# Kernel tuning notes

Measured on AMD Instinct MI355X. Metric: run time of the kernel, lower is better.

Reference implementation:

```python
import jax, jax.numpy as jnp
import numpy as np

ALPHA = 0.2          # LeakyReLU negative slope
WIN = 100            # window_size
D_EMBED = 2 * WIN    # default d_embed doubled in __init__


def setup_inputs() -> dict:
    key = jax.random.key(0)
    k1, k2, k3, k4 = jax.random.split(key, 4)
    B, W, F = 16, WIN, 128
    inp = jax.random.normal(k1, (B, W, F), dtype=jnp.float32)
    # linear: in=2*window_size, out=d_embed (stored as [in, out] for x @ W)
    lim = np.sqrt(1.0 / (2 * WIN))
    lin_w = jax.random.uniform(k2, (2 * WIN, D_EMBED), jnp.float32, -lim, lim)
    lin_b = jax.random.uniform(k3, (D_EMBED,), jnp.float32, -lim, lim)
    # attention vector w: [d_embed] (xavier on [d_embed,1])
    glim = np.sqrt(6.0 / (D_EMBED + 1))
    attn_w = jax.random.uniform(k4, (D_EMBED,), jnp.float32, -glim, glim)
    return {"input": inp, "lin_w": lin_w, "lin_b": lin_b, "attn_w": attn_w}


def reference(input, lin_w, lin_b, attn_w):
    # input: [B, window, features] -> x: [B, K, window] (K = features = nodes)
    x = jnp.transpose(input, (0, 2, 1))
    # Split the linear over the concat: linear(cat(xi, xj)) = xi@W1 + xj@W2 + b
    W1, W2 = lin_w[:WIN], lin_w[WIN:]          # each [window, d_embed]
    left = jnp.einsum("bkw,wd->bkd", x, W1)    # [B, K, d]
    right = jnp.einsum("bkw,wd->bkd", x, W2)   # [B, K, d]
    pre = left[:, :, None, :] + right[:, None, :, :] + lin_b  # [B, K, K, d]
    act = jnp.where(pre >= 0, pre, ALPHA * pre)                # LeakyReLU
    e = jnp.einsum("bijd,d->bij", act, attn_w)                 # [B, K, K]
    attention = jax.nn.softmax(e, axis=2)
    # dropout p=0.0 (eval/identity)
    h = jax.nn.sigmoid(jnp.einsum("bij,bjw->biw", attention, x))  # [B, K, window]
    return jnp.transpose(h, (0, 2, 1))  # [B, window, K]
```

## Files before the change

### kernel.cpp

```cpp
#include <hip/hip_runtime.h>

#define ALPHA 0.2f
#define BATCH 16
#define WIN 100
#define KN 128
#define DE 200
#define IT 8

typedef float v2f __attribute__((ext_vector_type(2)));

__global__ __launch_bounds__(256) void k_lin(
    const float* __restrict__ in, const float* __restrict__ lw,
    const float* __restrict__ lb, float* __restrict__ Rt, float* __restrict__ Lt) {
  int blk = blockIdx.x;
  int b = blk / 25, dt = blk % 25;
  int t = threadIdx.x;
  int j = t & (KN - 1);
  int dbase = __builtin_amdgcn_readfirstlane(dt * 8 + (t >> 7) * 4);
  const float* inb = in + (size_t)b * WIN * KN + j;
  const float* lwl = lw + dbase;
  const float* lwr = lw + WIN * DE + dbase;
  float la0 = 0, la1 = 0, la2 = 0, la3 = 0;
  float ra0 = 0, ra1 = 0, ra2 = 0, ra3 = 0;
#pragma unroll 10
  for (int w = 0; w < WIN; ++w) {
    float x = inb[w * KN];
    float4 wl = *reinterpret_cast<const float4*>(lwl + w * DE);
    float4 wr = *reinterpret_cast<const float4*>(lwr + w * DE);
    la0 = fmaf(x, wl.x, la0); la1 = fmaf(x, wl.y, la1);
    la2 = fmaf(x, wl.z, la2); la3 = fmaf(x, wl.w, la3);
    ra0 = fmaf(x, wr.x, ra0); ra1 = fmaf(x, wr.y, ra1);
    ra2 = fmaf(x, wr.z, ra2); ra3 = fmaf(x, wr.w, ra3);
  }
  float4 bb = *reinterpret_cast<const float4*>(lb + dbase);
  float* rp = Rt + ((size_t)b * DE + dbase) * KN + j;
  float* lp = Lt + ((size_t)b * DE + dbase) * KN + j;
  rp[0 * KN] = ra0 + bb.x; rp[1 * KN] = ra1 + bb.y;
  rp[2 * KN] = ra2 + bb.z; rp[3 * KN] = ra3 + bb.w;
  lp[0 * KN] = la0; lp[1 * KN] = la1; lp[2 * KN] = la2; lp[3 * KN] = la3;
}

__global__ __launch_bounds__(1024) void k_attn_out(
    const float* __restrict__ in, const float* __restrict__ aw,
    const float* __restrict__ Rt, const float* __restrict__ Lt,
    float* __restrict__ out) {
  int blk = blockIdx.x;
  int b = blk >> 4, it = blk & 15;
  int i0 = it * IT;
  int t = threadIdx.x;
  __shared__ float part[8][IT][KN];
  __shared__ float part_r[8][KN];
  __shared__ float ats[IT][132];

  {
    int j = t & (KN - 1);
    int db = __builtin_amdgcn_readfirstlane((t >> 7) * 25);
    int dh = t >> 7;
    const float* rtb = Rt + (size_t)b * DE * KN + j;
    const float* ltb = Lt + (size_t)b * DE * KN + i0;
    v2f acc0 = 0.f, acc1 = 0.f, acc2 = 0.f, acc3 = 0.f;
    float racc = 0.f;
#pragma unroll 5
    for (int dd = 0; dd < 25; ++dd) {
      int d = db + dd;
      float r = rtb[(size_t)d * KN];
      float a = aw[d];
      float4 L0 = *reinterpret_cast<const float4*>(ltb + (size_t)d * KN);
      float4 L1 = *reinterpret_cast<const float4*>(ltb + (size_t)d * KN + 4);
      racc = fmaf(r, a, racc);
      v2f rv = {r, r}, av = {a, a}, z = 0.f;
      v2f p0 = (v2f){L0.x, L0.y} + rv;
      v2f p1 = (v2f){L0.z, L0.w} + rv;
      v2f p2 = (v2f){L1.x, L1.y} + rv;
      v2f p3 = (v2f){L1.z, L1.w} + rv;
      p0 = __builtin_elementwise_min(p0, z);
      p1 = __builtin_elementwise_min(p1, z);
      p2 = __builtin_elementwise_min(p2, z);
      p3 = __builtin_elementwise_min(p3, z);
      acc0 += p0 * av; acc1 += p1 * av; acc2 += p2 * av; acc3 += p3 * av;
    }
    part[dh][0][j] = acc0.x; part[dh][1][j] = acc0.y;
    part[dh][2][j] = acc1.x; part[dh][3][j] = acc1.y;
    part[dh][4][j] = acc2.x; part[dh][5][j] = acc2.y;
    part[dh][6][j] = acc3.x; part[dh][7][j] = acc3.y;
    part_r[dh][j] = racc;
  }
  __syncthreads();

  {
    int wid = t >> 6;
    if (wid < IT) {
      int r = wid, l = t & 63;
      float ra0 = 0.f, ra1 = 0.f, m0 = 0.f, m1 = 0.f;
#pragma unroll
      for (int dh = 0; dh < 8; ++dh) {
        ra0 += part_r[dh][l];     ra1 += part_r[dh][l + 64];
        m0  += part[dh][r][l];    m1  += part[dh][r][l + 64];
      }
      float e0 = fmaf(m0, -(1.f - ALPHA), ra0);
      float e1 = fmaf(m1, -(1.f - ALPHA), ra1);
      float m = fmaxf(e0, e1);
      for (int off = 32; off; off >>= 1) m = fmaxf(m, __shfl_xor(m, off));
      float p0 = __expf(e0 - m), p1 = __expf(e1 - m);
      float s = p0 + p1;
      for (int off = 32; off; off >>= 1) s += __shfl_xor(s, off);
      float inv = 1.f / s;
      ats[r][l] = p0 * inv;
      ats[r][l + 64] = p1 * inv;
    }
  }
  __syncthreads();

  if (t < 4 * WIN) {
    int w = t >> 2, q = t & 3;
    const float* xw = in + ((size_t)b * WIN + w) * KN;
    const float* a0p = &ats[q * 2][0];
    const float* a1p = &ats[q * 2 + 1][0];
    float s0 = 0.f, s1 = 0.f;
#pragma unroll 8
    for (int j = 0; j < KN; j += 4) {
      float4 x4 = *reinterpret_cast<const float4*>(xw + j);
      float4 aa = *reinterpret_cast<const float4*>(a0p + j);
      float4 ab = *reinterpret_cast<const float4*>(a1p + j);
      s0 = fmaf(aa.x, x4.x, s0); s0 = fmaf(aa.y, x4.y, s0);
      s0 = fmaf(aa.z, x4.z, s0); s0 = fmaf(aa.w, x4.w, s0);
      s1 = fmaf(ab.x, x4.x, s1); s1 = fmaf(ab.y, x4.y, s1);
      s1 = fmaf(ab.z, x4.z, s1); s1 = fmaf(ab.w, x4.w, s1);
    }
    float o0 = 1.f / (1.f + __expf(-s0));
    float o1 = 1.f / (1.f + __expf(-s1));
    *reinterpret_cast<float2*>(&out[((size_t)b * WIN + w) * KN + i0 + q * 2]) =
        make_float2(o0, o1);
  }
}

extern "C" void kernel_launch(void* const* d_in, const int* in_sizes, int n_in,
                              void* d_out, int out_size, void* d_ws, size_t ws_size,
                              hipStream_t stream) {
  const float* in = (const float*)d_in[0];
  const float* lw = (const float*)d_in[1];
  const float* lb = (const float*)d_in[2];
  const float* aw = (const float*)d_in[3];
  float* out = (float*)d_out;

  float* Rt = (float*)d_ws;
  float* Lt = Rt + (size_t)BATCH * DE * KN;

  k_lin     <<<BATCH * 25, 256, 0, stream>>>(in, lw, lb, Rt, Lt);
  k_attn_out<<<BATCH * 16, 1024, 0, stream>>>(in, aw, Rt, Lt, out);
}
```

Measured before the change: 22.90 us.

## Split linear reduction across more threads and widen output stage parallelism

The linear kernel now runs 1024 threads per block. Each thread computes 2 output dims over half of the window, and the two partial sums are combined through shared memory before the stores. The attention kernel's d-loop is fully unrolled, and the output stage uses 800 threads computing one output each instead of 400 threads computing two. The goal is more threads in flight and shorter serial dependency chains, paid for with an extra shared-memory reduction and barrier, plus scalar stores in place of float2 stores.

Result: slower. 47.50 us (+107.4%).

```diff
diff --git a/kernel.cpp b/kernel.cpp
--- a/kernel.cpp
+++ b/kernel.cpp
@@ -9,35 +9,41 @@
 
 typedef float v2f __attribute__((ext_vector_type(2)));
 
-__global__ __launch_bounds__(256) void k_lin(
+__global__ __launch_bounds__(1024) void k_lin(
     const float* __restrict__ in, const float* __restrict__ lw,
     const float* __restrict__ lb, float* __restrict__ Rt, float* __restrict__ Lt) {
   int blk = blockIdx.x;
   int b = blk / 25, dt = blk % 25;
   int t = threadIdx.x;
   int j = t & (KN - 1);
-  int dbase = __builtin_amdgcn_readfirstlane(dt * 8 + (t >> 7) * 4);
-  const float* inb = in + (size_t)b * WIN * KN + j;
-  const float* lwl = lw + dbase;
-  const float* lwr = lw + WIN * DE + dbase;
-  float la0 = 0, la1 = 0, la2 = 0, la3 = 0;
-  float ra0 = 0, ra1 = 0, ra2 = 0, ra3 = 0;
-#pragma unroll 10
-  for (int w = 0; w < WIN; ++w) {
-    float x = inb[w * KN];
-    float4 wl = *reinterpret_cast<const float4*>(lwl + w * DE);
-    float4 wr = *reinterpret_cast<const float4*>(lwr + w * DE);
+  int g = t >> 7;
+  int dh = g & 3, wh = g >> 2;
+  int dp = __builtin_amdgcn_readfirstlane(dt * 8 + dh * 2);
+  __shared__ float pl[2][8][KN];
+  __shared__ float pr[2][8][KN];
+
+  const float* xp = in + ((size_t)b * WIN + wh * 50) * KN + j;
+  const float* lwl = lw + (size_t)(wh * 50) * DE + dp;
+  const float* lwr = lw + (size_t)(WIN + wh * 50) * DE + dp;
+  float la0 = 0, la1 = 0, ra0 = 0, ra1 = 0;
+#pragma unroll 25
+  for (int k = 0; k < 50; ++k) {
+    float x = xp[(size_t)k * KN];
+    float2 wl = *reinterpret_cast<const float2*>(lwl + (size_t)k * DE);
+    float2 wr = *reinterpret_cast<const float2*>(lwr + (size_t)k * DE);
     la0 = fmaf(x, wl.x, la0); la1 = fmaf(x, wl.y, la1);
-    la2 = fmaf(x, wl.z, la2); la3 = fmaf(x, wl.w, la3);
     ra0 = fmaf(x, wr.x, ra0); ra1 = fmaf(x, wr.y, ra1);
-    ra2 = fmaf(x, wr.z, ra2); ra3 = fmaf(x, wr.w, ra3);
   }
-  float4 bb = *reinterpret_cast<const float4*>(lb + dbase);
-  float* rp = Rt + ((size_t)b * DE + dbase) * KN + j;
-  float* lp = Lt + ((size_t)b * DE + dbase) * KN + j;
-  rp[0 * KN] = ra0 + bb.x; rp[1 * KN] = ra1 + bb.y;
-  rp[2 * KN] = ra2 + bb.z; rp[3 * KN] = ra3 + bb.w;
-  lp[0 * KN] = la0; lp[1 * KN] = la1; lp[2 * KN] = la2; lp[3 * KN] = la3;
+  pl[wh][dh * 2][j] = la0; pl[wh][dh * 2 + 1][j] = la1;
+  pr[wh][dh * 2][j] = ra0; pr[wh][dh * 2 + 1][j] = ra1;
+  __syncthreads();
+
+  int d8 = t >> 7;
+  int d = dt * 8 + d8;
+  float lsum = pl[0][d8][j] + pl[1][d8][j];
+  float rsum = pr[0][d8][j] + pr[1][d8][j] + lb[d];
+  Lt[((size_t)b * DE + d) * KN + j] = lsum;
+  Rt[((size_t)b * DE + d) * KN + j] = rsum;
 }
 
 __global__ __launch_bounds__(1024) void k_attn_out(
@@ -54,13 +60,13 @@
 
   {
     int j = t & (KN - 1);
-    int db = __builtin_amdgcn_readfirstlane((t >> 7) * 25);
     int dh = t >> 7;
+    int db = __builtin_amdgcn_readfirstlane(dh * 25);
     const float* rtb = Rt + (size_t)b * DE * KN + j;
     const float* ltb = Lt + (size_t)b * DE * KN + i0;
     v2f acc0 = 0.f, acc1 = 0.f, acc2 = 0.f, acc3 = 0.f;
     float racc = 0.f;
-#pragma unroll 5
+#pragma unroll 25
     for (int dd = 0; dd < 25; ++dd) {
       int d = db + dd;
       float r = rtb[(size_t)d * KN];
@@ -111,26 +117,19 @@
   }
   __syncthreads();
 
-  if (t < 4 * WIN) {
-    int w = t >> 2, q = t & 3;
+  if (t < 8 * WIN) {
+    int w = t >> 3, q = t & 7;
     const float* xw = in + ((size_t)b * WIN + w) * KN;
-    const float* a0p = &ats[q * 2][0];
-    const float* a1p = &ats[q * 2 + 1][0];
-    float s0 = 0.f, s1 = 0.f;
+    const float* ap = &ats[q][0];
+    float s = 0.f;
 #pragma unroll 8
-    for (int j = 0; j < KN; j += 4) {
-      float4 x4 = *reinterpret_cast<const float4*>(xw + j);
-      float4 aa = *reinterpret_cast<const float4*>(a0p + j);
-      float4 ab = *reinterpret_cast<const float4*>(a1p + j);
-      s0 = fmaf(aa.x, x4.x, s0); s0 = fmaf(aa.y, x4.y, s0);
-      s0 = fmaf(aa.z, x4.z, s0); s0 = fmaf(aa.w, x4.w, s0);
-      s1 = fmaf(ab.x, x4.x, s1); s1 = fmaf(ab.y, x4.y, s1);
-      s1 = fmaf(ab.z, x4.z, s1); s1 = fmaf(ab.w, x4.w, s1);
+    for (int jj = 0; jj < KN; jj += 4) {
+      float4 x4 = *reinterpret_cast<const float4*>(xw + jj);
+      float4 aa = *reinterpret_cast<const float4*>(ap + jj);
+      s = fmaf(aa.x, x4.x, s); s = fmaf(aa.y, x4.y, s);
+      s = fmaf(aa.z, x4.z, s); s = fmaf(aa.w, x4.w, s);
     }
-    float o0 = 1.f / (1.f + __expf(-s0));
-    float o1 = 1.f / (1.f + __expf(-s1));
-    *reinterpret_cast<float2*>(&out[((size_t)b * WIN + w) * KN + i0 + q * 2]) =
-        make_float2(o0, o1);
+    out[((size_t)b * WIN + w) * KN + i0 + q] = 1.f / (1.f + __expf(-s));
   }
 }
 
@@ -146,6 +145,6 @@
   float* Rt = (float*)d_ws;
   float* Lt = Rt + (size_t)BATCH * DE * KN;
 
-  k_lin     <<<BATCH * 25, 256, 0, stream>>>(in, lw, lb, Rt, Lt);
+  k_lin     <<<BATCH * 25, 1024, 0, stream>>>(in, lw, lb, Rt, Lt);
   k_attn_out<<<BATCH * 16, 1024, 0, stream>>>(in, aw, Rt, Lt, out);
 }
```
